# Performance work log

Hardware: AMD Instinct MI355X
Metric: run time of the kernel (lower is better)

## Reference

```python
import jax, jax.numpy as jnp
import numpy as np

B, C, H, W = 64, 16, 64, 64
NET = 16          # SpatialNN.net_size
S = C - 1         # number of SpatialNN steps in the ModuleList
LOG_2PI = float(np.log(2.0 * np.pi))


def _log_normal(x, loc, log_scale):
    # Normal(loc, exp(log_scale)).log_prob(x)
    z = (x - loc) * jnp.exp(-log_scale)
    return -0.5 * z * z - log_scale - 0.5 * LOG_2PI


def setup_inputs() -> dict:
    key = jax.random.key(0)
    ks = jax.random.split(key, 14)
    sc = 0.1
    samples = jax.random.normal(ks[0], (B, C, H, W), jnp.float32)
    n1_w1 = sc * jax.random.normal(ks[1], (NET, 1), jnp.float32)
    n1_b1 = sc * jax.random.normal(ks[2], (NET,), jnp.float32)
    n1_w2 = sc * jax.random.normal(ks[3], (NET, NET), jnp.float32)
    n1_b2 = sc * jax.random.normal(ks[4], (NET,), jnp.float32)
    n1_w3 = sc * jax.random.normal(ks[5], (2, NET), jnp.float32)
    n1_b3 = sc * jax.random.normal(ks[6], (2,), jnp.float32)
    # step s (s=0..S-1) consumes samples[:, :s+1]; pad conv1 weight to C input
    # channels with zeros in columns > s (identical math, enables fusion)
    w1 = sc * jax.random.normal(ks[7], (S, NET, C), jnp.float32)
    tri = (jnp.arange(C)[None, None, :] <= jnp.arange(S)[:, None, None]).astype(jnp.float32)
    w1 = w1 * tri
    b1 = sc * jax.random.normal(ks[8], (S, NET), jnp.float32)
    w2 = sc * jax.random.normal(ks[9], (S, NET, NET), jnp.float32)
    b2 = sc * jax.random.normal(ks[10], (S, NET), jnp.float32)
    w3 = sc * jax.random.normal(ks[11], (S, 2, NET), jnp.float32)
    b3 = sc * jax.random.normal(ks[12], (S, 2), jnp.float32)
    return {"samples": samples,
            "n1_w1": n1_w1, "n1_b1": n1_b1, "n1_w2": n1_w2, "n1_b2": n1_b2,
            "n1_w3": n1_w3, "n1_b3": n1_b3,
            "w1": w1, "b1": b1, "w2": w2, "b2": b2, "w3": w3, "b3": b3}


def reference(samples, n1_w1, n1_b1, n1_w2, n1_b2, n1_w3, n1_b3,
              w1, b1, w2, b2, w3, b3):
    # --- first channel: n1 applied to a zeros input (as in the torch code) ---
    x0 = jnp.zeros_like(samples[:, :1])                       # [B,1,H,W]
    h = jax.nn.relu(jnp.einsum('oc,bchw->bohw', n1_w1, x0) + n1_b1[:, None, None])
    h = jax.nn.relu(jnp.einsum('op,bphw->bohw', n1_w2, h) + n1_b2[:, None, None])
    p1 = jnp.einsum('op,bphw->bohw', n1_w3, h) + n1_b3[:, None, None]   # [B,2,H,W]
    lp1 = _log_normal(samples[:, 0], p1[:, 0], p1[:, 1])      # [B,H,W]

    h = jax.nn.relu(jnp.einsum('soc,bchw->bsohw', w1, samples)
                    + b1[None, :, :, None, None])             # [B,S,16,H,W]
    h = jax.nn.relu(jnp.einsum('sop,bsphw->bsohw', w2, h)
                    + b2[None, :, :, None, None])
    p = jnp.einsum('sop,bsphw->bsohw', w3, h) + b3[None, :, :, None, None]  # [B,S,2,H,W]
    lps = _log_normal(samples[:, 1:], p[:, :, 0], p[:, :, 1])  # [B,S,H,W]

    return lp1 + jnp.sum(lps, axis=1)                          # [B,H,W]
```

## Files before the change

### kernel.cpp

```cpp
#include <hip/hip_runtime.h>


#define NEG_HALF_LOG_2PI -0.91893853320467274f

typedef _Float16 f16x4 __attribute__((ext_vector_type(4)));
typedef __fp16   hf2   __attribute__((ext_vector_type(2)));
typedef float    f32x4 __attribute__((ext_vector_type(4)));

__device__ inline f16x4 pack_f16(f32x4 v) {
    hf2 p0 = __builtin_amdgcn_cvt_pkrtz(v[0], v[1]);
    hf2 p1 = __builtin_amdgcn_cvt_pkrtz(v[2], v[3]);
    f16x4 r;
    __builtin_memcpy(&r, &p0, 4);
    __builtin_memcpy((char*)&r + 4, &p1, 4);
    return r;
}

__device__ inline f16x4 relu_pack(f32x4 d) {
    hf2 p0 = __builtin_amdgcn_cvt_pkrtz(fmaxf(d[0], 0.0f), fmaxf(d[1], 0.0f));
    hf2 p1 = __builtin_amdgcn_cvt_pkrtz(fmaxf(d[2], 0.0f), fmaxf(d[3], 0.0f));
    f16x4 r;
    __builtin_memcpy(&r, &p0, 4);
    __builtin_memcpy((char*)&r + 4, &p1, 4);
    return r;
}

__global__ __launch_bounds__(256, 4) void spatial_main(
    const float* __restrict__ samples,
    const float* __restrict__ n1_b1,
    const float* __restrict__ n1_w2,
    const float* __restrict__ n1_b2,
    const float* __restrict__ n1_w3,
    const float* __restrict__ n1_b3,
    const float* __restrict__ w1,
    const float* __restrict__ b1,
    const float* __restrict__ w2,
    const float* __restrict__ b2,
    const float* __restrict__ w3,
    const float* __restrict__ b3,
    float* __restrict__ out)
{
    __shared__ _Float16 fA[45 * 256];
    __shared__ float    fC[15 * 2 * 16];

    const int tid   = threadIdx.x;
    const int lane  = tid & 63;
    const int wv    = tid >> 6;
    const int q     = lane >> 4;
    const int col   = lane & 15;
    const int lane4 = lane << 2;
    const int q4    = q << 2;
    const int roff  = col * 16 + q4;

    for (int j = tid; j < 30 * 64; j += 256) {
        int m   = j >> 6;
        int rem = j & 63;
        int r   = rem >> 2;
        int c   = rem & 3;
        const float* src = (m < 15) ? (w1 + m * 256) : (w2 + (m - 15) * 256);
        f32x4 v = *(const f32x4*)(src + r * 16 + (c << 2));
        int sl = (m < 15) ? (m * 3) : ((m - 15) * 3 + 1);
        *(f16x4*)&fA[sl * 256 + (((c << 4) + r) << 2)] = pack_f16(v);
    }
    for (int j = tid; j < 15 * 64; j += 256) {
        int s  = j >> 6;
        int ln = j & 63;
        int r  = ln & 15;
        int qq = ln >> 4;
        f32x4 v = {0.f, 0.f, 0.f, 0.f};
        if ((r & 3) < 2) v = *(const f32x4*)(w3 + s * 32 + ((r & 1) << 4) + (qq << 2));
        *(f16x4*)&fA[(s * 3 + 2) * 256 + (ln << 2)] = pack_f16(v);
    }
    for (int j = tid; j < 15 * 2 * 16; j += 256) {
        int s = j >> 5, layer = (j >> 4) & 1, o = j & 15;
        fC[j] = layer ? b2[s * 16 + o] : b1[s * 16 + o];
    }

    const int pbase = blockIdx.x * 256 + wv * 64;
    const int b     = pbase >> 12;
    const int hw    = pbase & 4095;
    const float* xw = samples + ((size_t)b << 16) + hw;

    f16x4 bx[4];
    #pragma unroll
    for (int ch = 0; ch < 4; ++ch)
        #pragma unroll
        for (int i = 0; i < 4; ++i)
            bx[ch][i] = (_Float16)xw[((q4 + i) << 12) + (ch << 4) + col];

    float xs[16];
    #pragma unroll
    for (int c = 0; c < 16; ++c)
        xs[c] = xw[(c << 12) + lane];

    float accz, accl;
    {
        f32x4 c1h = *(const f32x4*)(n1_b1 + q4);
        f16x4 h1h = relu_pack(c1h);
        f16x4 a2h = pack_f16(*(const f32x4*)(n1_w2 + roff));
        f32x4 c2h = *(const f32x4*)(n1_b2 + q4);
        f32x4 d2h = __builtin_amdgcn_mfma_f32_16x16x16f16(a2h, h1h, c2h, 0, 0, 0);
        f16x4 h2h = relu_pack(d2h);
        f32x4 v3h = {0.f, 0.f, 0.f, 0.f};
        if ((col & 3) < 2) v3h = *(const f32x4*)(n1_w3 + ((col & 1) << 4) + q4);
        f16x4 a3h = pack_f16(v3h);
        f32x4 c3h = {n1_b3[0], n1_b3[1], 0.0f, 0.0f};
        f32x4 d3h = __builtin_amdgcn_mfma_f32_16x16x16f16(a3h, h2h, c3h, 0, 0, 0);
        float ls = d3h[1];
        float z0 = (xs[0] - d3h[0]) * __expf(-ls);
        accz = z0 * z0;
        accl = ls;
    }

    __syncthreads();

    #pragma unroll
    for (int s = 0; s < 15; ++s) {
        f16x4 a1 = *(const f16x4*)&fA[(s * 3 + 0) * 256 + lane4];
        f16x4 a2 = *(const f16x4*)&fA[(s * 3 + 1) * 256 + lane4];
        f16x4 a3 = *(const f16x4*)&fA[(s * 3 + 2) * 256 + lane4];
        f32x4 c1 = *(const f32x4*)&fC[(s * 2 + 0) * 16 + q4];
        f32x4 c2 = *(const f32x4*)&fC[(s * 2 + 1) * 16 + q4];
        f32x4 c3 = {b3[s * 2 + 0], b3[s * 2 + 1], 0.0f, 0.0f};

        f32x4 d1[4];
        #pragma unroll
        for (int ch = 0; ch < 4; ++ch)
            d1[ch] = __builtin_amdgcn_mfma_f32_16x16x16f16(a1, bx[ch], c1, 0, 0, 0);
        f16x4 h1[4];
        #pragma unroll
        for (int ch = 0; ch < 4; ++ch)
            h1[ch] = relu_pack(d1[ch]);
        f32x4 d2[4];
        #pragma unroll
        for (int ch = 0; ch < 4; ++ch)
            d2[ch] = __builtin_amdgcn_mfma_f32_16x16x16f16(a2, h1[ch], c2, 0, 0, 0);
        f16x4 h2[4];
        #pragma unroll
        for (int ch = 0; ch < 4; ++ch)
            h2[ch] = relu_pack(d2[ch]);
        f32x4 d3[4];
        #pragma unroll
        for (int ch = 0; ch < 4; ++ch)
            d3[ch] = __builtin_amdgcn_mfma_f32_16x16x16f16(a3, h2[ch], c3, 0, 0, 0);

        float loc = q == 0 ? d3[0][0] : q == 1 ? d3[1][0] : q == 2 ? d3[2][0] : d3[3][0];
        float ls  = q == 0 ? d3[0][1] : q == 1 ? d3[1][1] : q == 2 ? d3[2][1] : d3[3][1];
        float z   = (xs[s + 1] - loc) * __expf(-ls);
        accz = fmaf(z, z, accz);
        accl += ls;
    }

    out[pbase + lane] = fmaf(-0.5f, accz, 16.0f * NEG_HALF_LOG_2PI - accl);
}

extern "C" void kernel_launch(void* const* d_in, const int* in_sizes, int n_in,
                              void* d_out, int out_size, void* d_ws, size_t ws_size,
                              hipStream_t stream) {
    const float* samples = (const float*)d_in[0];
    const float* n1_b1   = (const float*)d_in[2];
    const float* n1_w2   = (const float*)d_in[3];
    const float* n1_b2   = (const float*)d_in[4];
    const float* n1_w3   = (const float*)d_in[5];
    const float* n1_b3   = (const float*)d_in[6];
    const float* w1      = (const float*)d_in[7];
    const float* b1      = (const float*)d_in[8];
    const float* w2      = (const float*)d_in[9];
    const float* b2      = (const float*)d_in[10];
    const float* w3      = (const float*)d_in[11];
    const float* b3      = (const float*)d_in[12];
    float* out = (float*)d_out;

    spatial_main<<<dim3(1024), dim3(256), 0, stream>>>(
        samples, n1_b1, n1_w2, n1_b2, n1_w3, n1_b3,
        w1, b1, w2, b2, w3, b3, out);
}
```

Baseline: 103.7 us.

## Load per-step weights from global into registers instead of staging in LDS

Drops the shared-memory staging of all w1/w2/w3 and bias tiles, along with the block-wide barrier. Each wave now loads its MFMA A-fragments and bias vectors for the next step straight from global memory into registers, one step ahead, and converts them to f16 inside the loop. The aim is to cut the prologue cost, LDS traffic and synchronisation. The trade-off is repeated cached global loads and f16 conversions in every step, which adds latency exposure and register pressure. ReLU is also moved after the f16 pack so it uses a packed f16 max, and the w3 rows that were zero-padded now hold unused duplicates.

```diff
diff --git a/kernel.cpp b/kernel.cpp
--- a/kernel.cpp
+++ b/kernel.cpp
@@ -17,12 +17,13 @@
 }
 
 __device__ inline f16x4 relu_pack(f32x4 d) {
-    hf2 p0 = __builtin_amdgcn_cvt_pkrtz(fmaxf(d[0], 0.0f), fmaxf(d[1], 0.0f));
-    hf2 p1 = __builtin_amdgcn_cvt_pkrtz(fmaxf(d[2], 0.0f), fmaxf(d[3], 0.0f));
+    hf2 p0 = __builtin_amdgcn_cvt_pkrtz(d[0], d[1]);
+    hf2 p1 = __builtin_amdgcn_cvt_pkrtz(d[2], d[3]);
     f16x4 r;
     __builtin_memcpy(&r, &p0, 4);
     __builtin_memcpy((char*)&r + 4, &p1, 4);
-    return r;
+    const f16x4 z = {(_Float16)0, (_Float16)0, (_Float16)0, (_Float16)0};
+    return __builtin_elementwise_max(r, z);
 }
 
 __global__ __launch_bounds__(256, 4) void spatial_main(
@@ -40,41 +41,20 @@
     const float* __restrict__ b3,
     float* __restrict__ out)
 {
-    __shared__ _Float16 fA[45 * 256];
-    __shared__ float    fC[15 * 2 * 16];
-
     const int tid   = threadIdx.x;
     const int lane  = tid & 63;
     const int wv    = tid >> 6;
     const int q     = lane >> 4;
     const int col   = lane & 15;
-    const int lane4 = lane << 2;
     const int q4    = q << 2;
     const int roff  = col * 16 + q4;
+    const int w3off = ((col & 1) << 4) + q4;
 
-    for (int j = tid; j < 30 * 64; j += 256) {
-        int m   = j >> 6;
-        int rem = j & 63;
-        int r   = rem >> 2;
-        int c   = rem & 3;
-        const float* src = (m < 15) ? (w1 + m * 256) : (w2 + (m - 15) * 256);
-        f32x4 v = *(const f32x4*)(src + r * 16 + (c << 2));
-        int sl = (m < 15) ? (m * 3) : ((m - 15) * 3 + 1);
-        *(f16x4*)&fA[sl * 256 + (((c << 4) + r) << 2)] = pack_f16(v);
-    }
-    for (int j = tid; j < 15 * 64; j += 256) {
-        int s  = j >> 6;
-        int ln = j & 63;
-        int r  = ln & 15;
-        int qq = ln >> 4;
-        f32x4 v = {0.f, 0.f, 0.f, 0.f};
-        if ((r & 3) < 2) v = *(const f32x4*)(w3 + s * 32 + ((r & 1) << 4) + (qq << 2));
-        *(f16x4*)&fA[(s * 3 + 2) * 256 + (ln << 2)] = pack_f16(v);
-    }
-    for (int j = tid; j < 15 * 2 * 16; j += 256) {
-        int s = j >> 5, layer = (j >> 4) & 1, o = j & 15;
-        fC[j] = layer ? b2[s * 16 + o] : b1[s * 16 + o];
-    }
+    f32x4 ra1 = *(const f32x4*)(w1 + roff);
+    f32x4 ra2 = *(const f32x4*)(w2 + roff);
+    f32x4 ra3 = *(const f32x4*)(w3 + w3off);
+    f32x4 c1c = *(const f32x4*)(b1 + q4);
+    f32x4 c2c = *(const f32x4*)(b2 + q4);
 
     const int pbase = blockIdx.x * 256 + wv * 64;
     const int b     = pbase >> 12;
@@ -101,9 +81,7 @@
         f32x4 c2h = *(const f32x4*)(n1_b2 + q4);
         f32x4 d2h = __builtin_amdgcn_mfma_f32_16x16x16f16(a2h, h1h, c2h, 0, 0, 0);
         f16x4 h2h = relu_pack(d2h);
-        f32x4 v3h = {0.f, 0.f, 0.f, 0.f};
-        if ((col & 3) < 2) v3h = *(const f32x4*)(n1_w3 + ((col & 1) << 4) + q4);
-        f16x4 a3h = pack_f16(v3h);
+        f16x4 a3h = pack_f16(*(const f32x4*)(n1_w3 + w3off));
         f32x4 c3h = {n1_b3[0], n1_b3[1], 0.0f, 0.0f};
         f32x4 d3h = __builtin_amdgcn_mfma_f32_16x16x16f16(a3h, h2h, c3h, 0, 0, 0);
         float ls = d3h[1];
@@ -112,15 +90,21 @@
         accl = ls;
     }
 
-    __syncthreads();
-
     #pragma unroll
     for (int s = 0; s < 15; ++s) {
-        f16x4 a1 = *(const f16x4*)&fA[(s * 3 + 0) * 256 + lane4];
-        f16x4 a2 = *(const f16x4*)&fA[(s * 3 + 1) * 256 + lane4];
-        f16x4 a3 = *(const f16x4*)&fA[(s * 3 + 2) * 256 + lane4];
-        f32x4 c1 = *(const f32x4*)&fC[(s * 2 + 0) * 16 + q4];
-        f32x4 c2 = *(const f32x4*)&fC[(s * 2 + 1) * 16 + q4];
+        f16x4 a1 = pack_f16(ra1);
+        f16x4 a2 = pack_f16(ra2);
+        f16x4 a3 = pack_f16(ra3);
+        f32x4 c1 = c1c;
+        f32x4 c2 = c2c;
+
+        if (s < 14) {
+            ra1 = *(const f32x4*)(w1 + (s + 1) * 256 + roff);
+            ra2 = *(const f32x4*)(w2 + (s + 1) * 256 + roff);
+            ra3 = *(const f32x4*)(w3 + (s + 1) * 32 + w3off);
+            c1c = *(const f32x4*)(b1 + (s + 1) * 16 + q4);
+            c2c = *(const f32x4*)(b2 + (s + 1) * 16 + q4);
+        }
         f32x4 c3 = {b3[s * 2 + 0], b3[s * 2 + 1], 0.0f, 0.0f};
 
         f32x4 d1[4];
```

Measured after the change: 98.62 us. -4.9%, faster.
